# Performance work log

Measured on AMD Instinct MI355X. Metric: run time of the kernel, lower is better.

## Reference

```python
import jax, jax.numpy as jnp
import numpy as np

B, L, D, H = 2, 2048, 1024, 16
DK = D // H


def setup_inputs() -> dict:
    key = jax.random.key(0)
    ks = jax.random.split(key, 12)
    s = 1.0 / np.sqrt(D)
    inp = {
        "query": jax.random.normal(ks[0], (B, L, D), jnp.float32),
        "key_": jax.random.normal(ks[1], (B, L, D), jnp.float32),
        "value": jax.random.normal(ks[2], (B, L, D), jnp.float32),
        # causal boolean mask, broadcast over heads: (B, 1, L_q, L_k)
        "mask": jnp.broadcast_to(jnp.tril(jnp.ones((L, L), jnp.bool_)), (B, 1, L, L)),
        "w_q": jax.random.uniform(ks[3], (D, D), jnp.float32, -s, s),
        "b_q": jax.random.uniform(ks[4], (D,), jnp.float32, -s, s),
        "w_k": jax.random.uniform(ks[5], (D, D), jnp.float32, -s, s),
        "b_k": jax.random.uniform(ks[6], (D,), jnp.float32, -s, s),
        "w_v": jax.random.uniform(ks[7], (D, D), jnp.float32, -s, s),
        "b_v": jax.random.uniform(ks[8], (D,), jnp.float32, -s, s),
        "w_o": jax.random.uniform(ks[9], (D, D), jnp.float32, -s, s),
        "b_o": jax.random.uniform(ks[10], (D,), jnp.float32, -s, s),
    }
    return inp


def reference(query, key_, value, mask, w_q, b_q, w_k, b_k, w_v, b_v, w_o, b_o):
    # torch nn.Linear: y = x @ W.T + b, weight shape (out, in)
    Q = query @ w_q.T + b_q
    K = key_ @ w_k.T + b_k
    V = value @ w_v.T + b_v
    # (B, L, H, DK) -> (B, H, L, DK)
    Q = Q.reshape(B, L, H, DK).transpose(0, 2, 1, 3)
    K = K.reshape(B, L, H, DK).transpose(0, 2, 1, 3)
    V = V.reshape(B, L, H, DK).transpose(0, 2, 1, 3)
    scaling = jnp.sqrt(jnp.float32(DK))
    scores = jnp.einsum("bhqd,bhkd->bhqk", Q, K) / scaling  # (B,H,L,L)
    scores = jnp.where(mask, scores, jnp.float32(-1e9))
    attn = jax.nn.softmax(scores, axis=-1)
    out = jnp.einsum("bhqk,bhkd->bhqd", attn, V)  # (B,H,L,DK)
    out = out.transpose(0, 2, 1, 3).reshape(B, L, D)
    return out @ w_o.T + b_o
```

## Files before the change

### kernel.cpp

```cpp
#include <hip/hip_runtime.h>
#include <stdint.h>

#define Bb 2
#define Ll 2048
#define Dd 1024
#define Hh 16
#define DKd 64
#define Mm (Bb*Ll)

typedef __bf16 bf16_t;
typedef __bf16 bf16x8 __attribute__((ext_vector_type(8)));
typedef float f32x4 __attribute__((ext_vector_type(4)));
typedef unsigned u32x2 __attribute__((ext_vector_type(2)));

#define AS1C(p) ((const __attribute__((address_space(1))) void*)(p))
#define AS3(p)  ((__attribute__((address_space(3))) void*)(p))

__device__ __forceinline__ unsigned short bfu(float f){
  return __builtin_bit_cast(unsigned short, (bf16_t)f);
}
__device__ __forceinline__ void wait_vm6(){ asm volatile("s_waitcnt vmcnt(6)" ::: "memory"); }
__device__ __forceinline__ void wait_vm8(){ asm volatile("s_waitcnt vmcnt(8)" ::: "memory"); }
__device__ __forceinline__ void wait_vm0(){ asm volatile("s_waitcnt vmcnt(0)" ::: "memory"); }
__device__ __forceinline__ void bar(){
  __builtin_amdgcn_sched_barrier(0);
  __builtin_amdgcn_s_barrier();
  __builtin_amdgcn_sched_barrier(0);
}

struct Cvt7 { const float* in[7]; ushort4* out[7]; int n4[7]; };

__global__ void cvt_multi(Cvt7 a){
  const int z = blockIdx.y;
  int i = blockIdx.x*256 + threadIdx.x;
  if (i < a.n4[z]){
    float4 v = ((const float4*)a.in[z])[i];
    ushort4 o; o.x=bfu(v.x); o.y=bfu(v.y); o.z=bfu(v.z); o.w=bfu(v.w);
    a.out[z][i] = o;
  }
}

__global__ __launch_bounds__(256) void transpose_v(const bf16_t* __restrict__ Vh,
                                                   bf16_t* __restrict__ VT){
  __shared__ bf16_t Tl[64][72];
  const int bh = blockIdx.y;
  const int l0 = blockIdx.x * 64;
  const int tid = threadIdx.x;
  const bf16_t* src = Vh + (size_t)bh*Ll*DKd;
  bf16_t* dst = VT + (size_t)bh*Ll*DKd;
#pragma unroll
  for (int rd = 0; rd < 2; ++rd){
    int l = rd*32 + (tid>>3), dk0 = (tid&7)*8;
    bf16x8 v = *(const bf16x8*)(src + (size_t)(l0+l)*DKd + dk0);
#pragma unroll
    for (int j = 0; j < 8; ++j) Tl[dk0+j][l] = v[j];
  }
  __syncthreads();
#pragma unroll
  for (int rd = 0; rd < 2; ++rd){
    int dk = rd*32 + (tid>>3), lc = (tid&7)*8;
    *(bf16x8*)(dst + (size_t)dk*Ll + l0 + lc) = *(const bf16x8*)&Tl[dk][lc];
  }
}

#define BM 128
#define BN 64
#define BKs 64

struct GemmArgs {
  const bf16_t* A[3];
  const bf16_t* W[3];
  const float*  bias[3];
  void*         out[3];
  float         scale[3];
};

__device__ __forceinline__ void stage_tile(
    const bf16_t* __restrict__ A, const bf16_t* __restrict__ Bw,
    int m0, int n0, int K, int k0, bf16_t* As, bf16_t* Bs,
    int w, int srow, int scol)
{
#pragma unroll
  for (int i = 0; i < 4; i++) {
    int c = i*4 + w;
    int row = c*8 + srow;
    int sc = scol ^ ((row & 7) << 3);
    __builtin_amdgcn_global_load_lds(AS1C(A + (size_t)(m0+row)*K + k0 + sc),
                                     AS3(As + c*512), 16, 0, 0);
  }
#pragma unroll
  for (int i = 0; i < 2; i++) {
    int c = i*4 + w;
    int row = c*8 + srow;
    int sc = scol ^ ((row & 7) << 3);
    __builtin_amdgcn_global_load_lds(AS1C(Bw + (size_t)(n0+row)*K + k0 + sc),
                                     AS3(Bs + c*512), 16, 0, 0);
  }
}

template<int OUTMODE>
__global__ __launch_bounds__(256) void gemm_bt(GemmArgs ga, int M, int N, int K)
{
  const int z = blockIdx.z;
  const bf16_t* __restrict__ A  = ga.A[z];
  const bf16_t* __restrict__ Bw = ga.W[z];
  const float*  __restrict__ bias = ga.bias[z];
  void* __restrict__ out = ga.out[z];
  const float scale = ga.scale[z];

  __shared__ bf16_t As[2][BM*BKs];
  __shared__ bf16_t Bs[2][BN*BKs];
  const int tid = threadIdx.x;
  const int lane = tid & 63;
  const int w = tid >> 6;
  const int m0 = blockIdx.x * BM;
  const int n0 = blockIdx.y * BN;
  const int wr = (w >> 1) * 64, wc = (w & 1) * 32;
  const int lrow16 = lane & 15;
  const int kgrp = lane >> 4;
  const int srow = lane >> 3;
  const int scol = (lane & 7) * 8;

  f32x4 acc[4][2] = {};

  stage_tile(A, Bw, m0, n0, K, 0, As[0], Bs[0], w, srow, scol);

  const int KT = K / BKs;
  int cur = 0;
  for (int kt = 0; kt < KT; ++kt) {
    if (kt + 1 < KT) {
      stage_tile(A, Bw, m0, n0, K, (kt+1)*BKs, As[cur^1], Bs[cur^1], w, srow, scol);
      wait_vm6();
    } else {
      wait_vm0();
    }
    bar();
#pragma unroll
    for (int ks = 0; ks < 2; ++ks) {
      const int kbyte = ks*64 + kgrp*16;
      bf16x8 af[4], bfr[2];
#pragma unroll
      for (int m = 0; m < 4; m++) {
        int row = wr + m*16 + lrow16;
        af[m] = *(const bf16x8*)((const char*)As[cur] + row*128 + (kbyte ^ ((row & 7) << 4)));
      }
#pragma unroll
      for (int n = 0; n < 2; n++) {
        int row = wc + n*16 + lrow16;
        bfr[n] = *(const bf16x8*)((const char*)Bs[cur] + row*128 + (kbyte ^ ((row & 7) << 4)));
      }
#pragma unroll
      for (int m = 0; m < 4; m++)
#pragma unroll
        for (int n = 0; n < 2; n++)
          acc[m][n] = __builtin_amdgcn_mfma_f32_16x16x32_bf16(af[m], bfr[n], acc[m][n], 0, 0, 0);
    }
    bar();
    cur ^= 1;
  }

#pragma unroll
  for (int m = 0; m < 4; m++)
#pragma unroll
    for (int n = 0; n < 2; n++)
#pragma unroll
      for (int i = 0; i < 4; i++) {
        int row = m0 + wr + m*16 + kgrp*4 + i;
        int col = n0 + wc + n*16 + lrow16;
        float v = (acc[m][n][i] + bias[col]) * scale;
        if (OUTMODE == 1) {
          ((float*)out)[(size_t)row*N + col] = v;
        } else {
          int b = row >> 11, l = row & 2047;
          int h = col >> 6, dk = col & 63;
          ((unsigned short*)out)[((size_t)((b<<4) + h)*Ll + l)*DKd + dk] = bfu(v);
        }
      }
}

#define KVB 64

__global__ __launch_bounds__(128) void attn_kernel(
    const bf16_t* __restrict__ Qh, const bf16_t* __restrict__ Kh,
    const bf16_t* __restrict__ VTg, unsigned short* __restrict__ Oa)
{
  const int id = blockIdx.x;
  const int xcd = id & 7;
  const int hq  = (id >> 3) & 3;
  const int s5  = id >> 5;
  const int g2 = s5 >> 3, u = s5 & 7;
  int j;
  switch (g2) {
    case 0:  j = 31 - u; break;
    case 1:  j = u;      break;
    case 2:  j = 23 - u; break;
    default: j = 8 + u;  break;
  }
  const int bh = xcd + 8*hq;
  const int q0 = j * 64;
  const int nkv = j + 1;

  const int tid = threadIdx.x, lane = tid & 63, w = tid >> 6;
  const int r = lane & 15, g = lane >> 4;

  const bf16_t* Qp  = Qh  + (size_t)bh * Ll * DKd;
  const bf16_t* Kp  = Kh  + (size_t)bh * Ll * DKd;
  const bf16_t* VTp = VTg + (size_t)bh * Ll * DKd;

  __shared__ bf16_t Klds[2][64*64];
  __shared__ bf16_t Vlds[2][64*64];
  __shared__ bf16_t Plds[2][2][16*64];

  bf16x8 qf[2][2];
#pragma unroll
  for (int f = 0; f < 2; ++f)
#pragma unroll
    for (int ks = 0; ks < 2; ++ks)
      qf[f][ks] = *(const bf16x8*)(Qp + (size_t)(q0 + w*32 + f*16 + r)*DKd + ks*32 + g*8);

  bf16x8 ones;
#pragma unroll
  for (int jj = 0; jj < 8; ++jj) ones[jj] = (bf16_t)1.0f;

  f32x4 accO[2][4] = {};
  f32x4 accL[2] = {};
  float mrow[2] = {-1e30f, -1e30f};

  const int krow_l = lane >> 3;
  const int kcol_l = ((lane & 7)*16) ^ (krow_l << 4);
  char* Pw0 = (char*)&Plds[w][0][0];
  char* Pw1 = (char*)&Plds[w][1][0];
  const int rsw = (r & 7) << 4;
  const int b_ = bh >> 4, h_ = bh & 15;

  auto pre_tiles = [&](int kv, int buf){
#pragma unroll
    for (int i = 0; i < 4; ++i) {
      int c = i*2 + w;
      __builtin_amdgcn_global_load_lds(
        AS1C((const char*)Kp + (size_t)(kv*KVB + c*8 + krow_l)*128 + kcol_l),
        AS3((char*)&Klds[buf][0] + c*1024), 16, 0, 0);
      __builtin_amdgcn_global_load_lds(
        AS1C((const char*)VTp + (size_t)(c*8 + krow_l)*4096 + kv*128 + kcol_l),
        AS3((char*)&Vlds[buf][0] + c*1024), 16, 0, 0);
    }
  };

  pre_tiles(0, 0);

  int cur = 0;
  for (int s = 0; s < nkv; ++s) {
    if (s + 1 < nkv) {
      pre_tiles(s + 1, cur^1);
      wait_vm8();
    } else {
      wait_vm0();
    }
    bar();

    const char* Kbase = (const char*)&Klds[cur][0];
    f32x4 sv[2][4] = {};
    __builtin_amdgcn_s_setprio(1);
#pragma unroll
    for (int ks = 0; ks < 2; ++ks) {
      const int kbyte = ks*64 + g*16;
#pragma unroll
      for (int n = 0; n < 4; ++n) {
        int row = n*16 + r;
        bf16x8 kf = *(const bf16x8*)(Kbase + row*128 + (kbyte ^ ((row & 7) << 4)));
        sv[0][n] = __builtin_amdgcn_mfma_f32_16x16x32_bf16(kf, qf[0][ks], sv[0][n], 0, 0, 0);
        sv[1][n] = __builtin_amdgcn_mfma_f32_16x16x32_bf16(kf, qf[1][ks], sv[1][n], 0, 0, 0);
      }
    }
    __builtin_amdgcn_s_setprio(0);

    if (s == nkv - 1) {
      const int kv0 = s * KVB;
#pragma unroll
      for (int f = 0; f < 2; ++f) {
        const int qg = q0 + w*32 + f*16 + r;
#pragma unroll
        for (int n = 0; n < 4; ++n)
#pragma unroll
          for (int i = 0; i < 4; ++i)
            if (kv0 + n*16 + g*4 + i > qg) sv[f][n][i] = -1e30f;
      }
    }

#pragma unroll
    for (int f = 0; f < 2; ++f) {
      float m0 = fmaxf(fmaxf(sv[f][0][0], sv[f][0][1]), sv[f][0][2]);
      float m1 = fmaxf(fmaxf(sv[f][0][3], sv[f][1][0]), sv[f][1][1]);
      float m2 = fmaxf(fmaxf(sv[f][1][2], sv[f][1][3]), sv[f][2][0]);
      float m3 = fmaxf(fmaxf(sv[f][2][1], sv[f][2][2]), sv[f][2][3]);
      float m4 = fmaxf(fmaxf(sv[f][3][0], sv[f][3][1]), sv[f][3][2]);
      float mx = fmaxf(fmaxf(fmaxf(m0, m1), m2), fmaxf(fmaxf(m3, m4), sv[f][3][3]));
      if (__any(mx > mrow[f] + 8.f)) {
        mx = fmaxf(mx, __shfl_xor(mx, 16));
        mx = fmaxf(mx, __shfl_xor(mx, 32));
        float mnew = fmaxf(mrow[f], mx);
        float corr = __builtin_amdgcn_exp2f(mrow[f] - mnew);
        float c0 = __shfl(corr, g*4 + 0);
        float c1 = __shfl(corr, g*4 + 1);
        float c2 = __shfl(corr, g*4 + 2);
        float c3 = __shfl(corr, g*4 + 3);
#pragma unroll
        for (int n = 0; n < 4; ++n) {
          accO[f][n][0] *= c0; accO[f][n][1] *= c1;
          accO[f][n][2] *= c2; accO[f][n][3] *= c3;
        }
        accL[f][0] *= c0; accL[f][1] *= c1; accL[f][2] *= c2; accL[f][3] *= c3;
        mrow[f] = mnew;
      }
#pragma unroll
      for (int n = 0; n < 4; ++n)
#pragma unroll
        for (int i = 0; i < 4; ++i)
          sv[f][n][i] = __builtin_amdgcn_exp2f(sv[f][n][i] - mrow[f]);

      char* Pw = f ? Pw1 : Pw0;
#pragma unroll
      for (int n = 0; n < 4; ++n) {
        unsigned lo = (unsigned)bfu(sv[f][n][0]) | ((unsigned)bfu(sv[f][n][1]) << 16);
        unsigned hi = (unsigned)bfu(sv[f][n][2]) | ((unsigned)bfu(sv[f][n][3]) << 16);
        u32x2 pk; pk[0] = lo; pk[1] = hi;
        *(u32x2*)(Pw + r*128 + ((n*32 + g*8) ^ rsw)) = pk;
      }
    }

    const char* Vbase = (const char*)&Vlds[cur][0];
    __builtin_amdgcn_s_setprio(1);
#pragma unroll
    for (int ks = 0; ks < 2; ++ks) {
      const int kbyte = ks*64 + g*16;
      bf16x8 pa0 = *(const bf16x8*)(Pw0 + r*128 + (kbyte ^ rsw));
      bf16x8 pa1 = *(const bf16x8*)(Pw1 + r*128 + (kbyte ^ rsw));
      accL[0] = __builtin_amdgcn_mfma_f32_16x16x32_bf16(pa0, ones, accL[0], 0, 0, 0);
      accL[1] = __builtin_amdgcn_mfma_f32_16x16x32_bf16(pa1, ones, accL[1], 0, 0, 0);
#pragma unroll
      for (int n = 0; n < 4; ++n) {
        int row = n*16 + r;
        bf16x8 vf = *(const bf16x8*)(Vbase + row*128 + (kbyte ^ ((row & 7) << 4)));
        accO[0][n] = __builtin_amdgcn_mfma_f32_16x16x32_bf16(pa0, vf, accO[0][n], 0, 0, 0);
        accO[1][n] = __builtin_amdgcn_mfma_f32_16x16x32_bf16(pa1, vf, accO[1][n], 0, 0, 0);
      }
    }
    __builtin_amdgcn_s_setprio(0);

    bar();
    cur ^= 1;
  }

#pragma unroll
  for (int f = 0; f < 2; ++f)
#pragma unroll
    for (int i = 0; i < 4; ++i) {
      float inv = 1.f / accL[f][i];
      int q = q0 + w*32 + f*16 + g*4 + i;
#pragma unroll
      for (int n = 0; n < 4; ++n)
        Oa[((size_t)(b_*Ll + q))*Dd + h_*DKd + n*16 + r] = bfu(accO[f][n][i] * inv);
    }
}

extern "C" void kernel_launch(void* const* d_in, const int* in_sizes, int n_in,
                              void* d_out, int out_size, void* d_ws, size_t ws_size,
                              hipStream_t stream)
{
  const float* q  = (const float*)d_in[0];
  const float* k  = (const float*)d_in[1];
  const float* v  = (const float*)d_in[2];
  const float* wq = (const float*)d_in[4];
  const float* bq = (const float*)d_in[5];
  const float* wk = (const float*)d_in[6];
  const float* bk = (const float*)d_in[7];
  const float* wv = (const float*)d_in[8];
  const float* bv = (const float*)d_in[9];
  const float* wo = (const float*)d_in[10];
  const float* bo = (const float*)d_in[11];

  char* ws = (char*)d_ws;
  bf16_t* Xq = (bf16_t*)(ws + 0);
  bf16_t* Xk = (bf16_t*)(ws + 8388608);
  bf16_t* Xv = (bf16_t*)(ws + 16777216);
  bf16_t* Wq = (bf16_t*)(ws + 25165824);
  bf16_t* Wk = (bf16_t*)(ws + 27262976);
  bf16_t* Wv = (bf16_t*)(ws + 29360128);
  bf16_t* Wo = (bf16_t*)(ws + 31457280);
  bf16_t* Qh = (bf16_t*)(ws + 33554432);
  bf16_t* Kh = (bf16_t*)(ws + 41943040);
  bf16_t* Vh = (bf16_t*)(ws + 50331648);
  bf16_t* Oa = (bf16_t*)(ws + 58720256);
  bf16_t* VT = Xq;

  const int NX4 = Mm * Dd / 4;
  const int NW4 = Dd * Dd / 4;

  Cvt7 cv;
  cv.in[0]=q;  cv.out[0]=(ushort4*)Xq; cv.n4[0]=NX4;
  cv.in[1]=k;  cv.out[1]=(ushort4*)Xk; cv.n4[1]=NX4;
  cv.in[2]=v;  cv.out[2]=(ushort4*)Xv; cv.n4[2]=NX4;
  cv.in[3]=wq; cv.out[3]=(ushort4*)Wq; cv.n4[3]=NW4;
  cv.in[4]=wk; cv.out[4]=(ushort4*)Wk; cv.n4[4]=NW4;
  cv.in[5]=wv; cv.out[5]=(ushort4*)Wv; cv.n4[5]=NW4;
  cv.in[6]=wo; cv.out[6]=(ushort4*)Wo; cv.n4[6]=NW4;
  cvt_multi<<<dim3(NX4/256, 7), 256, 0, stream>>>(cv);

  const float qscale = 0.125f * 1.4426950408889634f;
  GemmArgs gqkv;
  gqkv.A[0]=Xq; gqkv.A[1]=Xk; gqkv.A[2]=Xv;
  gqkv.W[0]=Wq; gqkv.W[1]=Wk; gqkv.W[2]=Wv;
  gqkv.bias[0]=bq; gqkv.bias[1]=bk; gqkv.bias[2]=bv;
  gqkv.out[0]=Qh; gqkv.out[1]=Kh; gqkv.out[2]=Vh;
  gqkv.scale[0]=qscale; gqkv.scale[1]=1.0f; gqkv.scale[2]=1.0f;
  gemm_bt<0><<<dim3(Mm/BM, Dd/BN, 3), 256, 0, stream>>>(gqkv, Mm, Dd, Dd);

  transpose_v<<<dim3(32, 32), 256, 0, stream>>>(Vh, VT);

  attn_kernel<<<dim3(1024), 128, 0, stream>>>(Qh, Kh, VT, (unsigned short*)Oa);

  GemmArgs go;
  go.A[0]=Oa; go.A[1]=Oa; go.A[2]=Oa;
  go.W[0]=Wo; go.W[1]=Wo; go.W[2]=Wo;
  go.bias[0]=bo; go.bias[1]=bo; go.bias[2]=bo;
  go.out[0]=d_out; go.out[1]=d_out; go.out[2]=d_out;
  go.scale[0]=1.0f; go.scale[1]=1.0f; go.scale[2]=1.0f;
  gemm_bt<1><<<dim3(Mm/BM, Dd/BN, 1), 256, 0, stream>>>(go, Mm, Dd, Dd);
}
```

Before: 129.7 us.

## Pair causal query tiles per block to balance attention work

Each attention block now handles two query tiles, j and 31-j, so every block runs exactly 33 KV steps instead of a variable j+1. The grid halves from 1024 to 512 blocks, and the K/V prefetch pipeline carries across the tile switch, with the first tile's output written and the second tile's Q reloaded mid-loop. This replaces the earlier hand-ordered schedule meant to ease causal load imbalance. The cost is fewer blocks in flight for latency hiding and extra state resets in the loop.

New measurement: 140.3 us. 1.08x slower.

```diff
diff --git a/kernel.cpp b/kernel.cpp
--- a/kernel.cpp
+++ b/kernel.cpp
@@ -187,18 +187,10 @@
   const int id = blockIdx.x;
   const int xcd = id & 7;
   const int hq  = (id >> 3) & 3;
-  const int s5  = id >> 5;
-  const int g2 = s5 >> 3, u = s5 & 7;
-  int j;
-  switch (g2) {
-    case 0:  j = 31 - u; break;
-    case 1:  j = u;      break;
-    case 2:  j = 23 - u; break;
-    default: j = 8 + u;  break;
-  }
-  const int bh = xcd + 8*hq;
-  const int q0 = j * 64;
-  const int nkv = j + 1;
+  const int j   = id >> 5;
+  const int bh  = xcd + 8*hq;
+  const int sA  = j;
+  const int qtB = 31 - j;
 
   const int tid = threadIdx.x, lane = tid & 63, w = tid >> 6;
   const int r = lane & 15, g = lane >> 4;
@@ -211,6 +203,7 @@
   __shared__ bf16_t Vlds[2][64*64];
   __shared__ bf16_t Plds[2][2][16*64];
 
+  int q0 = j * 64;
   bf16x8 qf[2][2];
 #pragma unroll
   for (int f = 0; f < 2; ++f)
@@ -249,14 +242,17 @@
   pre_tiles(0, 0);
 
   int cur = 0;
-  for (int s = 0; s < nkv; ++s) {
-    if (s + 1 < nkv) {
-      pre_tiles(s + 1, cur^1);
+  for (int s = 0; s < 33; ++s) {
+    if (s < 32) {
+      int kv2 = (s < sA) ? s + 1 : s - sA;
+      pre_tiles(kv2, cur^1);
       wait_vm8();
     } else {
       wait_vm0();
     }
     bar();
+
+    const int kv0 = ((s <= sA) ? s : s - sA - 1) * KVB;
 
     const char* Kbase = (const char*)&Klds[cur][0];
     f32x4 sv[2][4] = {};
@@ -274,8 +270,7 @@
     }
     __builtin_amdgcn_s_setprio(0);
 
-    if (s == nkv - 1) {
-      const int kv0 = s * KVB;
+    if (s == sA || s == 32) {
 #pragma unroll
       for (int f = 0; f < 2; ++f) {
         const int qg = q0 + w*32 + f*16 + r;
@@ -347,6 +342,30 @@
     }
     __builtin_amdgcn_s_setprio(0);
 
+    if (s == sA) {
+#pragma unroll
+      for (int f = 0; f < 2; ++f)
+#pragma unroll
+        for (int i = 0; i < 4; ++i) {
+          float inv = 1.f / accL[f][i];
+          int q = q0 + w*32 + f*16 + g*4 + i;
+#pragma unroll
+          for (int n = 0; n < 4; ++n)
+            Oa[((size_t)(b_*Ll + q))*Dd + h_*DKd + n*16 + r] = bfu(accO[f][n][i] * inv);
+        }
+      q0 = qtB * 64;
+#pragma unroll
+      for (int f = 0; f < 2; ++f) {
+#pragma unroll
+        for (int ks = 0; ks < 2; ++ks)
+          qf[f][ks] = *(const bf16x8*)(Qp + (size_t)(q0 + w*32 + f*16 + r)*DKd + ks*32 + g*8);
+        accO[f][0] = f32x4{}; accO[f][1] = f32x4{};
+        accO[f][2] = f32x4{}; accO[f][3] = f32x4{};
+        accL[f] = f32x4{};
+        mrow[f] = -1e30f;
+      }
+    }
+
     bar();
     cur ^= 1;
   }
@@ -417,7 +436,7 @@
 
   transpose_v<<<dim3(32, 32), 256, 0, stream>>>(Vh, VT);
 
-  attn_kernel<<<dim3(1024), 128, 0, stream>>>(Qh, Kh, VT, (unsigned short*)Oa);
+  attn_kernel<<<dim3(512), 128, 0, stream>>>(Qh, Kh, VT, (unsigned short*)Oa);
 
   GemmArgs go;
   go.A[0]=Oa; go.A[1]=Oa; go.A[2]=Oa;
```
